# Kernel tuning notes

Hardware: AMD Instinct MI355X
Metric: run time of the kernel (lower is better)

## Reference

```python
import jax, jax.numpy as jnp
import numpy as np

N_NODES = 50000
N_EDGES = 500000
F = 128
AVG_DEG_LOG = float(np.log(11.0))  # log(avg_degree + 1), avg_degree = 10


def setup_inputs() -> dict:
    key = jax.random.key(0)
    ks = jax.random.split(key, 40)
    inp = {
        "x": jax.random.normal(ks[0], (N_NODES, F), dtype=jnp.float32),
        "edge_index": jax.random.randint(ks[1], (2, N_EDGES), 0, N_NODES, dtype=jnp.int32),
    }
    k = 2
    for i in range(5):
        inp[f"pre_w{i}"] = 0.05 * jax.random.normal(ks[k], (F, 2 * F), dtype=jnp.float32); k += 1
        inp[f"pre_b{i}"] = jnp.zeros((F,), jnp.float32)
        inp[f"adl{i}"] = jnp.full((1,), AVG_DEG_LOG, jnp.float32)
        inp[f"post_w{i}"] = 0.05 * jax.random.normal(ks[k], (F, 13 * F), dtype=jnp.float32); k += 1
        inp[f"post_b{i}"] = jnp.zeros((F,), jnp.float32)
        inp[f"lin_w{i}"] = 0.05 * jax.random.normal(ks[k], (F, F), dtype=jnp.float32); k += 1
        inp[f"lin_b{i}"] = jnp.zeros((F,), jnp.float32)
    return inp


def _pna_layer(x, src, dst, deg, adl, pre_w, pre_b, post_w, post_b, lin_w, lin_b):
    n = x.shape[0]
    # message: pre_nn(cat([x_i, x_j]))  -> [E, F]
    h = jnp.concatenate([x[dst], x[src]], axis=-1)        # [E, 2F]
    m = h @ pre_w.T + pre_b                               # [E, F]
    # multi-aggregator scatter-reduce onto target nodes
    inv = (1.0 / jnp.maximum(deg, 1.0))[:, None]
    mean = jax.ops.segment_sum(m, dst, num_segments=n) * inv
    mean2 = jax.ops.segment_sum(m * m, dst, num_segments=n) * inv
    std = jnp.sqrt(jnp.maximum(mean2 - mean * mean, 0.0) + 1e-5)
    has = (deg > 0)[:, None]
    mn = jnp.where(has, jax.ops.segment_min(m, dst, num_segments=n), 0.0)
    mx = jnp.where(has, jax.ops.segment_max(m, dst, num_segments=n), 0.0)
    agg = jnp.concatenate([mean, mn, mx, std], axis=-1)   # [N, 4F]
    # degree scalers: identity / amplification / attenuation
    scale = (jnp.log(jnp.maximum(deg, 1.0) + 1.0) / adl)[:, None]  # [N,1]
    out = jnp.concatenate([x, agg, agg * scale, agg / scale], axis=-1)  # [N, 13F]
    out = out @ post_w.T + post_b                          # [N, F]
    return out @ lin_w.T + lin_b                           # [N, F]


def reference(x, edge_index,
              pre_w0, pre_b0, adl0, post_w0, post_b0, lin_w0, lin_b0,
              pre_w1, pre_b1, adl1, post_w1, post_b1, lin_w1, lin_b1,
              pre_w2, pre_b2, adl2, post_w2, post_b2, lin_w2, lin_b2,
              pre_w3, pre_b3, adl3, post_w3, post_b3, lin_w3, lin_b3,
              pre_w4, pre_b4, adl4, post_w4, post_b4, lin_w4, lin_b4):
    src, dst = edge_index[0], edge_index[1]
    n = x.shape[0]
    deg = jax.ops.segment_sum(jnp.ones(src.shape[0], x.dtype), dst, num_segments=n)
    layers = [
        (pre_w0, pre_b0, adl0, post_w0, post_b0, lin_w0, lin_b0),
        (pre_w1, pre_b1, adl1, post_w1, post_b1, lin_w1, lin_b1),
        (pre_w2, pre_b2, adl2, post_w2, post_b2, lin_w2, lin_b2),
        (pre_w3, pre_b3, adl3, post_w3, post_b3, lin_w3, lin_b3),
        (pre_w4, pre_b4, adl4, post_w4, post_b4, lin_w4, lin_b4),
    ]
    h = x
    for pw, pb, adl, ow, ob, lw, lb in layers:
        h = _pna_layer(h, src, dst, deg, adl, pw, pb, ow, ob, lw, lb)
        h = jax.nn.relu(h)
    return h
```

## Files before the change

### kernel.cpp

```cpp
#include <hip/hip_runtime.h>

typedef short bf16x8 __attribute__((ext_vector_type(8)));
typedef float f32x4 __attribute__((ext_vector_type(4)));

struct Ptr5 { const float* p[5]; };
struct UPtr5 { unsigned char* p[5]; };
struct FPtr5 { float* p[5]; };

__device__ __forceinline__ unsigned short f2bf(float f) {
  unsigned u = __float_as_uint(f);
  u += 0x7fffu + ((u >> 16) & 1u);
  return (unsigned short)(u >> 16);
}

__device__ __forceinline__ float bf2f(unsigned short h) {
  return __uint_as_float(((unsigned)h) << 16);
}

__device__ __forceinline__ void gload16(const void* g, void* l) {
  __builtin_amdgcn_global_load_lds((const __attribute__((address_space(1))) void*)g,
                                   (__attribute__((address_space(3))) void*)l, 16, 0, 0);
}

__device__ __forceinline__ bf16x8 rf64(const unsigned char* lds, int row, int pb) {
  return *(const bf16x8*)(lds + row * 64 + (pb ^ ((((row) >> 1) & 3) << 4)));
}
__device__ __forceinline__ bf16x8 rf256(const unsigned char* lds, int row, int pb) {
  return *(const bf16x8*)(lds + row * 256 + (pb ^ ((row & 7) << 4)));
}

__global__ void k_hist(const int* __restrict__ dst, int* __restrict__ deg, int E) {
  int e = blockIdx.x * blockDim.x + threadIdx.x;
  if (e < E) atomicAdd(&deg[dst[e]], 1);
}

__global__ __launch_bounds__(256) void k_scan_part(const int* __restrict__ deg,
                                                    int* __restrict__ bsum, int n) {
  int b = blockIdx.x, t = threadIdx.x;
  int base = b * 1024 + t * 4;
  int s = 0;
#pragma unroll
  for (int i = 0; i < 4; i++) {
    int idx = base + i;
    if (idx < n) s += deg[idx];
  }
  for (int off = 1; off < 64; off <<= 1) s += __shfl_xor(s, off);
  __shared__ int ws[4];
  if ((t & 63) == 0) ws[t >> 6] = s;
  __syncthreads();
  if (t == 0) bsum[b] = ws[0] + ws[1] + ws[2] + ws[3];
}

__global__ void k_scan_bsum(const int* __restrict__ bsum, int* __restrict__ boff,
                            int* __restrict__ row_start, int nb, int n) {
  int t = threadIdx.x;
  int orig = (t < nb) ? bsum[t] : 0;
  int v = orig;
  for (int off = 1; off < 64; off <<= 1) {
    int u = __shfl_up(v, off);
    if (t >= off) v += u;
  }
  if (t < nb) boff[t] = v - orig;
  if (t == nb - 1) row_start[n] = v;
}

__global__ __launch_bounds__(256) void k_scan_final(const int* __restrict__ deg,
                                                     const int* __restrict__ boff,
                                                     int* __restrict__ row_start,
                                                     int* __restrict__ cursor, int n) {
  int b = blockIdx.x, t = threadIdx.x;
  int lane = t & 63, wid = t >> 6;
  int base = b * 1024 + t * 4;
  int v[4];
  int s = 0;
#pragma unroll
  for (int i = 0; i < 4; i++) {
    int idx = base + i;
    v[i] = (idx < n) ? deg[idx] : 0;
    s += v[i];
  }
  int sc = s;
  for (int off = 1; off < 64; off <<= 1) {
    int u = __shfl_up(sc, off);
    if (lane >= off) sc += u;
  }
  __shared__ int ws[4];
  if (lane == 63) ws[wid] = sc;
  __syncthreads();
  int wbase = 0;
  for (int i = 0; i < wid; i++) wbase += ws[i];
  int run = boff[b] + wbase + sc - s;
#pragma unroll
  for (int i = 0; i < 4; i++) {
    int idx = base + i;
    if (idx < n) {
      row_start[idx] = run;
      cursor[idx] = run;
      run += v[i];
    }
  }
}

__global__ void k_scatter(const int* __restrict__ src, const int* __restrict__ dst,
                          int* __restrict__ cursor, int* __restrict__ edge_src, int E) {
  int e = blockIdx.x * blockDim.x + threadIdx.x;
  if (e < E) {
    int pos = atomicAdd(&cursor[dst[e]], 1);
    edge_src[pos] = src[e];
  }
}

__global__ void k_cast(const float* __restrict__ x, unsigned short* __restrict__ X, int n) {
  int i = blockIdx.x * blockDim.x + threadIdx.x;
  if (i >= n * 32) return;
  int r = i >> 5, c = (i & 31) * 4;
  float4 v = *(const float4*)(x + (size_t)r * 128 + c);
  ushort4 o;
  o.x = f2bf(v.x); o.y = f2bf(v.y); o.z = f2bf(v.z); o.w = f2bf(v.w);
  *(ushort4*)(X + (size_t)r * 640 + c) = o;
}

__global__ __launch_bounds__(256) void k_fold5(Ptr5 post_w, Ptr5 pre_w, Ptr5 pre_b,
                                                Ptr5 post_b, float* __restrict__ Whg_base,
                                                FPtr5 biasg) {
  int L = blockIdx.y;
  int id = blockIdx.x * blockDim.x + threadIdx.x;
  if (id >= 3 * 128 * 128) return;
  int g = id >> 14;
  int rem = id & 16383;
  int j = rem >> 7, k = rem & 127;
  const float* pw = post_w.p[L] + j * 1664 + g * 512 + 128;
  const float* prw = pre_w.p[L];
  float acc = 0.f, bacc = 0.f;
  for (int f = 0; f < 128; f++) {
    float wc = pw[f] + pw[128 + f] + pw[256 + f];
    acc += wc * prw[f * 256 + k];
    if (k == 0) bacc += wc * pre_b.p[L][f];
  }
  Whg_base[L * 49152 + id] = acc;
  if (k == 0) biasg.p[L][g * 128 + j] = bacc + ((g == 0) ? post_b.p[L][j] : 0.f);
}

__global__ void k_repack_post5(Ptr5 post_w, const float* __restrict__ Whg_base, UPtr5 img) {
  int L = blockIdx.y;
  int i = blockIdx.x * blockDim.x + threadIdx.x;
  if (i >= 384 * 640) return;
  const float* pwL = post_w.p[L];
  const float* Whg = Whg_base + L * 49152;
  unsigned char* im = img.p[L];
  int r = i / 640, k = i - r * 640;
  int g = r >> 7, jj = r & 127;
  float v;
  if (k < 128) v = ((g == 0) ? pwL[jj * 1664 + k] : 0.0f) + Whg[(g * 128 + jj) * 128 + k];
  else v = pwL[jj * 1664 + g * 512 + 128 + (k - 128)];
  int kt = k >> 5, kl = k & 31;
  int ch = kl >> 3, e = kl & 7;
  int off = kt * 24576 + r * 64 + ((ch ^ ((r >> 1) & 3)) << 4) + e * 2;
  *(unsigned short*)(im + off) = f2bf(v);
}

__global__ void k_repack_ql5(Ptr5 pre_w, Ptr5 lin_w, UPtr5 qimg, UPtr5 limg) {
  int L = blockIdx.y;
  int which = blockIdx.z;
  int i = blockIdx.x * blockDim.x + threadIdx.x;
  if (i >= 128 * 128) return;
  int j = i >> 7, k = i & 127;
  float v = which ? lin_w.p[L][i] : pre_w.p[L][j * 256 + 128 + k];
  unsigned char* im = which ? limg.p[L] : qimg.p[L];
  int ch = k >> 3, e = k & 7;
  int off = j * 256 + ((ch * 16) ^ ((j & 7) << 4)) + e * 2;
  *(unsigned short*)(im + off) = f2bf(v);
}

__global__ __launch_bounds__(512, 2) void k_gemm1(const unsigned short* __restrict__ X,
                                                   const unsigned char* __restrict__ Qimg,
                                                   unsigned short* __restrict__ Qb) {
  __shared__ __align__(16) unsigned char lds[65536];
  int tid = threadIdx.x;
  int w = tid >> 6, lane = tid & 63;
  int wr = w >> 2, wc = w & 3;
  int l16 = lane & 15, lhi = lane >> 4;
  int row0 = blockIdx.x * 128;
  const char* Xb = (const char*)X;
#pragma unroll
  for (int j = 0; j < 4; j++) {
    int off = w * 4096 + j * 1024 + lane * 16;
    int r = off >> 8, pos = off & 255;
    int ch = (pos ^ ((r & 7) << 4)) >> 4;
    gload16(Xb + (size_t)(row0 + r) * 1280 + ch * 16, lds + w * 4096 + j * 1024);
  }
#pragma unroll
  for (int j = 0; j < 4; j++) {
    int off = w * 4096 + j * 1024;
    gload16(Qimg + off + lane * 16, lds + 32768 + off);
  }
  __syncthreads();
  f32x4 acc[4][2];
#pragma unroll
  for (int m = 0; m < 4; m++)
#pragma unroll
    for (int j = 0; j < 2; j++) acc[m][j] = (f32x4){0.f, 0.f, 0.f, 0.f};
#pragma unroll
  for (int ks = 0; ks < 4; ks++) {
    int pb = ks * 64 + lhi * 16;
    bf16x8 af[4], bfr[2];
#pragma unroll
    for (int m = 0; m < 4; m++) af[m] = rf256(lds, wr * 64 + m * 16 + l16, pb);
#pragma unroll
    for (int j = 0; j < 2; j++) bfr[j] = rf256(lds + 32768, wc * 32 + j * 16 + l16, pb);
#pragma unroll
    for (int m = 0; m < 4; m++)
#pragma unroll
      for (int j = 0; j < 2; j++)
        acc[m][j] = __builtin_amdgcn_mfma_f32_16x16x32_bf16(af[m], bfr[j], acc[m][j], 0, 0, 0);
  }
#pragma unroll
  for (int m = 0; m < 4; m++)
#pragma unroll
    for (int j = 0; j < 2; j++)
#pragma unroll
      for (int i = 0; i < 4; i++) {
        int r = row0 + wr * 64 + m * 16 + lhi * 4 + i;
        int c = wc * 32 + j * 16 + l16;
        Qb[(size_t)r * 128 + c] = f2bf(acc[m][j][i]);
      }
}

__global__ __launch_bounds__(256) void k_agg(const unsigned short* __restrict__ Qb,
                                              const int* __restrict__ row_start,
                                              const int* __restrict__ edge_src,
                                              const unsigned short* __restrict__ X_h,
                                              const float* __restrict__ pre_w,
                                              const float* __restrict__ pre_b,
                                              const float* __restrict__ adl,
                                              unsigned short* __restrict__ X,
                                              float* __restrict__ scale,
                                              float* __restrict__ inv_scale, int n) {
  int wv = (blockIdx.x * blockDim.x + threadIdx.x) >> 6;
  int lane = threadIdx.x & 63;
  int half = lane >> 5, fl = lane & 31;
  int v = 2 * wv + half;
  if (v >= n) return;
  int r0 = row_start[v], r1 = row_start[v + 1];
  int dg = r1 - r0;
  float mean[4], mnv[4], mxv[4], sdv[4];
  if (dg > 0) {
    float s[4] = {0.f, 0.f, 0.f, 0.f}, q[4] = {0.f, 0.f, 0.f, 0.f};
    float mn[4], mx[4];
#pragma unroll
    for (int t = 0; t < 4; t++) { mn[t] = INFINITY; mx[t] = -INFINITY; }
    const unsigned char* qbase = (const unsigned char*)Qb;
#define ACC4(U)                                                              \
  do {                                                                       \
    float f0 = __uint_as_float((U).x << 16);                                 \
    float f1 = __uint_as_float((U).x & 0xffff0000u);                         \
    float f2 = __uint_as_float((U).y << 16);                                 \
    float f3 = __uint_as_float((U).y & 0xffff0000u);                         \
    s[0] += f0; s[1] += f1; s[2] += f2; s[3] += f3;                          \
    q[0] += f0 * f0; q[1] += f1 * f1; q[2] += f2 * f2; q[3] += f3 * f3;      \
    mn[0] = fminf(mn[0], f0); mn[1] = fminf(mn[1], f1);                      \
    mn[2] = fminf(mn[2], f2); mn[3] = fminf(mn[3], f3);                      \
    mx[0] = fmaxf(mx[0], f0); mx[1] = fmaxf(mx[1], f1);                      \
    mx[2] = fmaxf(mx[2], f2); mx[3] = fmaxf(mx[3], f3);                      \
  } while (0)
    int e = r0;
    for (; e + 3 < r1; e += 4) {
      int sa = edge_src[e], sb = edge_src[e + 1], sc = edge_src[e + 2], sd = edge_src[e + 3];
      uint2 ua = *(const uint2*)(qbase + (size_t)sa * 256 + 8 * fl);
      uint2 ub = *(const uint2*)(qbase + (size_t)sb * 256 + 8 * fl);
      uint2 uc = *(const uint2*)(qbase + (size_t)sc * 256 + 8 * fl);
      uint2 ud = *(const uint2*)(qbase + (size_t)sd * 256 + 8 * fl);
      ACC4(ua); ACC4(ub); ACC4(uc); ACC4(ud);
    }
    for (; e < r1; e++) {
      int sa = edge_src[e];
      uint2 ua = *(const uint2*)(qbase + (size_t)sa * 256 + 8 * fl);
      ACC4(ua);
    }
#undef ACC4
    float invd = 1.0f / (float)dg;
#pragma unroll
    for (int t = 0; t < 4; t++) {
      mean[t] = s[t] * invd;
      float var = fmaxf(q[t] * invd - mean[t] * mean[t], 0.f);
      sdv[t] = sqrtf(var + 1e-5f);
      mnv[t] = mn[t]; mxv[t] = mx[t];
    }
  } else {
    const unsigned short* hv = X_h + (size_t)v * 640;
#pragma unroll
    for (int t = 0; t < 4; t++) {
      int j = 4 * fl + t;
      float c = pre_b[j];
      for (int k = 0; k < 128; k++) c += bf2f(hv[k]) * pre_w[j * 256 + k];
      mean[t] = mnv[t] = mxv[t] = -c;
      sdv[t] = sqrtf(1e-5f);
    }
  }
  unsigned short* row = X + (size_t)v * 640 + 128;
  ushort4 wm, wn, wx, ws;
  wm.x = f2bf(mean[0]); wm.y = f2bf(mean[1]); wm.z = f2bf(mean[2]); wm.w = f2bf(mean[3]);
  wn.x = f2bf(mnv[0]);  wn.y = f2bf(mnv[1]);  wn.z = f2bf(mnv[2]);  wn.w = f2bf(mnv[3]);
  wx.x = f2bf(mxv[0]);  wx.y = f2bf(mxv[1]);  wx.z = f2bf(mxv[2]);  wx.w = f2bf(mxv[3]);
  ws.x = f2bf(sdv[0]);  ws.y = f2bf(sdv[1]);  ws.z = f2bf(sdv[2]);  ws.w = f2bf(sdv[3]);
  *(ushort4*)(row + 4 * fl) = wm;
  *(ushort4*)(row + 128 + 4 * fl) = wn;
  *(ushort4*)(row + 256 + 4 * fl) = wx;
  *(ushort4*)(row + 384 + 4 * fl) = ws;
  if (fl == 0) {
    float degf = (float)dg;
    float sc = logf(fmaxf(degf, 1.0f) + 1.0f) / adl[0];
    scale[v] = sc;
    inv_scale[v] = 1.0f / sc;
  }
}

__global__ __launch_bounds__(512, 2) void k_fused(const unsigned short* __restrict__ X,
                                                   const unsigned char* __restrict__ Bimg,
                                                   const unsigned char* __restrict__ Limg,
                                                   const unsigned char* __restrict__ Qimg,
                                                   const float* __restrict__ scale,
                                                   const float* __restrict__ invs,
                                                   const float* __restrict__ biasg,
                                                   const float* __restrict__ lin_b,
                                                   unsigned short* __restrict__ Xh,
                                                   unsigned short* __restrict__ Qb,
                                                   float* __restrict__ Fout,
                                                   int M, int write_f32, int doC) {
  __shared__ __align__(16) unsigned char lds[65536];
  int tid = threadIdx.x;
  int w = tid >> 6, lane = tid & 63;
  int wr = w >> 2, wc = w & 3;
  int l16 = lane & 15, lhi = lane >> 4;
  int row0 = blockIdx.x * 128;
  const char* Xb = (const char*)X;
  int ra = tid >> 2;
  int posa = (((tid & 3) ^ ((ra >> 1) & 3)) << 4);
  const char* srcA = Xb + (size_t)(row0 + ra) * 1280 + posa;
  unsigned dstA = tid * 16;
  const unsigned char* srcB = Bimg + tid * 16;
  unsigned dstB = 8192 + tid * 16;

  f32x4 acc[4][6];
#pragma unroll
  for (int m = 0; m < 4; m++)
#pragma unroll
    for (int f = 0; f < 6; f++) acc[m][f] = (f32x4){0.f, 0.f, 0.f, 0.f};

#define STAGE_AB(buf, kt)                                                          \
  do {                                                                             \
    unsigned base = (buf) * 32768u;                                                \
    gload16(srcA + (kt) * 64, lds + base + dstA);                                  \
    _Pragma("unroll") for (int j = 0; j < 3; j++)                                  \
        gload16(srcB + (size_t)(kt) * 24576 + j * 8192, lds + base + dstB + j * 8192); \
  } while (0)

#define COMPUTE_A(buf)                                                             \
  do {                                                                             \
    const unsigned char* LA = lds + (buf) * 32768u;                                \
    const unsigned char* LB = LA + 8192;                                           \
    int pb = lhi * 16;                                                             \
    bf16x8 af[4], bfr[6];                                                          \
    _Pragma("unroll") for (int m = 0; m < 4; m++)                                  \
        af[m] = rf64(LA, wr * 64 + m * 16 + l16, pb);                              \
    _Pragma("unroll") for (int f = 0; f < 6; f++)                                  \
        bfr[f] = rf64(LB, (f >> 1) * 128 + wc * 32 + (f & 1) * 16 + l16, pb);      \
    _Pragma("unroll") for (int m = 0; m < 4; m++)                                  \
        _Pragma("unroll") for (int f = 0; f < 6; f++)                              \
            acc[m][f] =                                                            \
                __builtin_amdgcn_mfma_f32_16x16x32_bf16(af[m], bfr[f], acc[m][f], 0, 0, 0); \
  } while (0)

  STAGE_AB(0, 0);
  STAGE_AB(1, 1);
  for (int kt = 0; kt < 20; kt++) {
    if (kt < 19) {
      asm volatile("s_waitcnt vmcnt(4)" ::: "memory");
    } else {
      asm volatile("s_waitcnt vmcnt(0)" ::: "memory");
    }
    __builtin_amdgcn_s_barrier();
    __builtin_amdgcn_sched_barrier(0);
    __builtin_amdgcn_s_setprio(1);
    COMPUTE_A(kt & 1);
    __builtin_amdgcn_s_setprio(0);
    __builtin_amdgcn_sched_barrier(0);
    __builtin_amdgcn_s_barrier();
    if (kt < 18) STAGE_AB(kt & 1, kt + 2);
  }

#pragma unroll
  for (int j = 0; j < 4; j++) {
    int off = w * 4096 + j * 1024;
    gload16(Limg + off + lane * 16, lds + off);
  }
#pragma unroll
  for (int m = 0; m < 4; m++)
#pragma unroll
    for (int i = 0; i < 4; i++) {
      int rl = wr * 64 + m * 16 + lhi * 4 + i;
      int r = row0 + rl;
      float s = scale[r], iv = invs[r];
      int swz = (rl & 7) << 4;
#pragma unroll
      for (int j = 0; j < 2; j++) {
        int c = wc * 32 + j * 16 + l16;
        float v = acc[m][j][i] + s * acc[m][2 + j][i] + iv * acc[m][4 + j][i] + biasg[c] +
                  s * biasg[128 + c] + iv * biasg[256 + c];
        *(unsigned short*)(lds + 32768 + rl * 256 + ((2 * c) ^ swz)) = f2bf(v);
      }
    }
  __syncthreads();

  f32x4 acc2[4][2];
#pragma unroll
  for (int m = 0; m < 4; m++)
#pragma unroll
    for (int j = 0; j < 2; j++) acc2[m][j] = (f32x4){0.f, 0.f, 0.f, 0.f};
#pragma unroll
  for (int ks = 0; ks < 4; ks++) {
    int pb = ks * 64 + lhi * 16;
    bf16x8 af[4], bfr[2];
#pragma unroll
    for (int m = 0; m < 4; m++) af[m] = rf256(lds + 32768, wr * 64 + m * 16 + l16, pb);
#pragma unroll
    for (int j = 0; j < 2; j++) bfr[j] = rf256(lds, wc * 32 + j * 16 + l16, pb);
#pragma unroll
    for (int m = 0; m < 4; m++)
#pragma unroll
      for (int j = 0; j < 2; j++)
        acc2[m][j] = __builtin_amdgcn_mfma_f32_16x16x32_bf16(af[m], bfr[j], acc2[m][j], 0, 0, 0);
  }
  __syncthreads();

  if (doC) {
#pragma unroll
    for (int j = 0; j < 4; j++) {
      int off = w * 4096 + j * 1024;
      gload16(Qimg + off + lane * 16, lds + off);
    }
  }
#pragma unroll
  for (int m = 0; m < 4; m++)
#pragma unroll
    for (int j = 0; j < 2; j++)
#pragma unroll
      for (int i = 0; i < 4; i++) {
        int rl = wr * 64 + m * 16 + lhi * 4 + i;
        int r = row0 + rl;
        int c = wc * 32 + j * 16 + l16;
        float v = fmaxf(acc2[m][j][i] + lin_b[c], 0.0f);
        unsigned short hb = f2bf(v);
        Xh[(size_t)r * 640 + c] = hb;
        if (doC) *(unsigned short*)(lds + 32768 + rl * 256 + ((2 * c) ^ ((rl & 7) << 4))) = hb;
        if (write_f32 && r < M) Fout[(size_t)r * 128 + c] = v;
      }
  if (!doC) return;
  __syncthreads();

  f32x4 acc3[4][2];
#pragma unroll
  for (int m = 0; m < 4; m++)
#pragma unroll
    for (int j = 0; j < 2; j++) acc3[m][j] = (f32x4){0.f, 0.f, 0.f, 0.f};
#pragma unroll
  for (int ks = 0; ks < 4; ks++) {
    int pb = ks * 64 + lhi * 16;
    bf16x8 af[4], bfr[2];
#pragma unroll
    for (int m = 0; m < 4; m++) af[m] = rf256(lds + 32768, wr * 64 + m * 16 + l16, pb);
#pragma unroll
    for (int j = 0; j < 2; j++) bfr[j] = rf256(lds, wc * 32 + j * 16 + l16, pb);
#pragma unroll
    for (int m = 0; m < 4; m++)
#pragma unroll
      for (int j = 0; j < 2; j++)
        acc3[m][j] = __builtin_amdgcn_mfma_f32_16x16x32_bf16(af[m], bfr[j], acc3[m][j], 0, 0, 0);
  }
#pragma unroll
  for (int m = 0; m < 4; m++)
#pragma unroll
    for (int j = 0; j < 2; j++)
#pragma unroll
      for (int i = 0; i < 4; i++) {
        int r = row0 + wr * 64 + m * 16 + lhi * 4 + i;
        int c = wc * 32 + j * 16 + l16;
        Qb[(size_t)r * 128 + c] = f2bf(acc3[m][j][i]);
      }
#undef STAGE_AB
#undef COMPUTE_A
}

extern "C" void kernel_launch(void* const* d_in, const int* in_sizes, int n_in,
                              void* d_out, int out_size, void* d_ws, size_t ws_size,
                              hipStream_t stream) {
  const float* x = (const float*)d_in[0];
  const int* eidx = (const int*)d_in[1];
  int n = in_sizes[0] / 128;
  int E = in_sizes[1] / 2;
  int n_pad = (n + 127) & ~127;
  const int* src = eidx;
  const int* dst = eidx + E;

  Ptr5 pre_w, pre_b, adl, post_w, post_b, lin_w, lin_b;
  for (int i = 0; i < 5; i++) {
    pre_w.p[i] = (const float*)d_in[2 + i * 7 + 0];
    pre_b.p[i] = (const float*)d_in[2 + i * 7 + 1];
    adl.p[i] = (const float*)d_in[2 + i * 7 + 2];
    post_w.p[i] = (const float*)d_in[2 + i * 7 + 3];
    post_b.p[i] = (const float*)d_in[2 + i * 7 + 4];
    lin_w.p[i] = (const float*)d_in[2 + i * 7 + 5];
    lin_b.p[i] = (const float*)d_in[2 + i * 7 + 6];
  }

  char* ws = (char*)d_ws;
  size_t off = 0;
  auto alloc = [&](size_t bytes) {
    char* p = ws + off;
    off += (bytes + 255) & ~(size_t)255;
    return p;
  };
  unsigned short* X = (unsigned short*)alloc((size_t)n_pad * 640 * 2);
  unsigned short* Qb = (unsigned short*)alloc((size_t)n_pad * 128 * 2);
  float* scale = (float*)alloc((size_t)n_pad * 4);
  float* invs = (float*)alloc((size_t)n_pad * 4);
  int* deg = (int*)alloc((size_t)n * 4);
  int* row_start = (int*)alloc((size_t)(n + 1) * 4);
  int* cursor = (int*)alloc((size_t)n * 4);
  int* edge_src = (int*)alloc((size_t)E * 4);
  int nb = (n + 1023) / 1024;
  int* bsum = (int*)alloc((size_t)nb * 4);
  int* boff = (int*)alloc((size_t)nb * 4);
  float* Whg_base = (float*)alloc((size_t)5 * 3 * 128 * 128 * 4);
  UPtr5 Bpost, Lin, Qimg;
  FPtr5 biasg;
  for (int i = 0; i < 5; i++) {
    Bpost.p[i] = (unsigned char*)alloc(491520);
    Lin.p[i] = (unsigned char*)alloc(32768);
    Qimg.p[i] = (unsigned char*)alloc(32768);
    biasg.p[i] = (float*)alloc(384 * 4);
  }

  hipMemsetAsync(deg, 0, (size_t)n * 4, stream);
  k_hist<<<(E + 255) / 256, 256, 0, stream>>>(dst, deg, E);
  k_scan_part<<<nb, 256, 0, stream>>>(deg, bsum, n);
  k_scan_bsum<<<1, 64, 0, stream>>>(bsum, boff, row_start, nb, n);
  k_scan_final<<<nb, 256, 0, stream>>>(deg, boff, row_start, cursor, n);
  k_scatter<<<(E + 255) / 256, 256, 0, stream>>>(src, dst, cursor, edge_src, E);
  k_cast<<<(n * 32 + 255) / 256, 256, 0, stream>>>(x, X, n);
  k_fold5<<<dim3(192, 5), 256, 0, stream>>>(post_w, pre_w, pre_b, post_b, Whg_base, biasg);
  k_repack_post5<<<dim3(960, 5), 256, 0, stream>>>(post_w, Whg_base, Bpost);
  k_repack_ql5<<<dim3(64, 5, 2), 256, 0, stream>>>(pre_w, lin_w, Qimg, Lin);

  int gblocks = n_pad / 128;
  k_gemm1<<<gblocks, 512, 0, stream>>>(X, Qimg.p[0], Qb);
  for (int L = 0; L < 5; L++) {
    k_agg<<<(n + 7) / 8, 256, 0, stream>>>(Qb, row_start, edge_src, X, pre_w.p[L], pre_b.p[L],
                                           adl.p[L], X, scale, invs, n);
    k_fused<<<gblocks, 512, 0, stream>>>(X, Bpost.p[L], Lin.p[L],
                                         (L < 4) ? Qimg.p[L + 1] : Qimg.p[0], scale, invs,
                                         biasg.p[L], lin_b.p[L], X, Qb, (float*)d_out, n,
                                         (L == 4) ? 1 : 0, (L < 4) ? 1 : 0);
  }
}
```

Measured before the change: 501.6 us.

## Load GEMM operands directly from global into registers, repacking B per-lane

Replaces the LDS double-buffered global_load_lds pipeline in the fused kernel's main GEMM with direct per-lane global loads of A and B fragments into registers. It removes the barriers, waitcnts and LDS traffic. The post-weight image is re-laid out so that each lane's 16-byte B fragment is contiguous in MFMA-fragment order. The trade-off is that B is no longer shared through LDS: every wave reloads its fragments from global/L2, and there is no explicit prefetch to hide latency.

After: 665.8 us. +32.7%, slower.

```diff
diff --git a/kernel.cpp b/kernel.cpp
--- a/kernel.cpp
+++ b/kernel.cpp
@@ -22,9 +22,6 @@
                                    (__attribute__((address_space(3))) void*)l, 16, 0, 0);
 }
 
-__device__ __forceinline__ bf16x8 rf64(const unsigned char* lds, int row, int pb) {
-  return *(const bf16x8*)(lds + row * 64 + (pb ^ ((((row) >> 1) & 3) << 4)));
-}
 __device__ __forceinline__ bf16x8 rf256(const unsigned char* lds, int row, int pb) {
   return *(const bf16x8*)(lds + row * 256 + (pb ^ ((row & 7) << 4)));
 }
@@ -145,18 +142,22 @@
   int L = blockIdx.y;
   int i = blockIdx.x * blockDim.x + threadIdx.x;
   if (i >= 384 * 640) return;
-  const float* pwL = post_w.p[L];
+  int chunk = i >> 9;
+  int rem = i & 511;
+  int f = chunk % 6;
+  int wcc = (chunk / 6) & 3;
+  int kt = chunk / 24;
+  int l16 = rem >> 5;
+  int lhi = (rem >> 3) & 3;
+  int e = rem & 7;
+  int row = (f >> 1) * 128 + wcc * 32 + (f & 1) * 16 + l16;
+  int k = kt * 32 + lhi * 8 + e;
+  int g = row >> 7, jj = row & 127;
   const float* Whg = Whg_base + L * 49152;
-  unsigned char* im = img.p[L];
-  int r = i / 640, k = i - r * 640;
-  int g = r >> 7, jj = r & 127;
   float v;
-  if (k < 128) v = ((g == 0) ? pwL[jj * 1664 + k] : 0.0f) + Whg[(g * 128 + jj) * 128 + k];
-  else v = pwL[jj * 1664 + g * 512 + 128 + (k - 128)];
-  int kt = k >> 5, kl = k & 31;
-  int ch = kl >> 3, e = kl & 7;
-  int off = kt * 24576 + r * 64 + ((ch ^ ((r >> 1) & 3)) << 4) + e * 2;
-  *(unsigned short*)(im + off) = f2bf(v);
+  if (k < 128) v = ((g == 0) ? post_w.p[L][jj * 1664 + k] : 0.0f) + Whg[(g * 128 + jj) * 128 + k];
+  else v = post_w.p[L][jj * 1664 + g * 512 + 128 + (k - 128)];
+  ((unsigned short*)img.p[L])[i] = f2bf(v);
 }
 
 __global__ void k_repack_ql5(Ptr5 pre_w, Ptr5 lin_w, UPtr5 qimg, UPtr5 limg) {
@@ -333,13 +334,13 @@
   int wr = w >> 2, wc = w & 3;
   int l16 = lane & 15, lhi = lane >> 4;
   int row0 = blockIdx.x * 128;
-  const char* Xb = (const char*)X;
-  int ra = tid >> 2;
-  int posa = (((tid & 3) ^ ((ra >> 1) & 3)) << 4);
-  const char* srcA = Xb + (size_t)(row0 + ra) * 1280 + posa;
-  unsigned dstA = tid * 16;
-  const unsigned char* srcB = Bimg + tid * 16;
-  unsigned dstB = 8192 + tid * 16;
+  const unsigned char* Xb = (const unsigned char*)X;
+
+  const unsigned char* Ab[4];
+#pragma unroll
+  for (int m = 0; m < 4; m++)
+    Ab[m] = Xb + (size_t)(row0 + wr * 64 + m * 16 + l16) * 1280 + lhi * 16;
+  const unsigned char* Bb = Bimg + wc * 6144 + l16 * 64 + lhi * 16;
 
   f32x4 acc[4][6];
 #pragma unroll
@@ -347,46 +348,18 @@
 #pragma unroll
     for (int f = 0; f < 6; f++) acc[m][f] = (f32x4){0.f, 0.f, 0.f, 0.f};
 
-#define STAGE_AB(buf, kt)                                                          \
-  do {                                                                             \
-    unsigned base = (buf) * 32768u;                                                \
-    gload16(srcA + (kt) * 64, lds + base + dstA);                                  \
-    _Pragma("unroll") for (int j = 0; j < 3; j++)                                  \
-        gload16(srcB + (size_t)(kt) * 24576 + j * 8192, lds + base + dstB + j * 8192); \
-  } while (0)
-
-#define COMPUTE_A(buf)                                                             \
-  do {                                                                             \
-    const unsigned char* LA = lds + (buf) * 32768u;                                \
-    const unsigned char* LB = LA + 8192;                                           \
-    int pb = lhi * 16;                                                             \
-    bf16x8 af[4], bfr[6];                                                          \
-    _Pragma("unroll") for (int m = 0; m < 4; m++)                                  \
-        af[m] = rf64(LA, wr * 64 + m * 16 + l16, pb);                              \
-    _Pragma("unroll") for (int f = 0; f < 6; f++)                                  \
-        bfr[f] = rf64(LB, (f >> 1) * 128 + wc * 32 + (f & 1) * 16 + l16, pb);      \
-    _Pragma("unroll") for (int m = 0; m < 4; m++)                                  \
-        _Pragma("unroll") for (int f = 0; f < 6; f++)                              \
-            acc[m][f] =                                                            \
-                __builtin_amdgcn_mfma_f32_16x16x32_bf16(af[m], bfr[f], acc[m][f], 0, 0, 0); \
-  } while (0)
-
-  STAGE_AB(0, 0);
-  STAGE_AB(1, 1);
+#pragma unroll
   for (int kt = 0; kt < 20; kt++) {
-    if (kt < 19) {
-      asm volatile("s_waitcnt vmcnt(4)" ::: "memory");
-    } else {
-      asm volatile("s_waitcnt vmcnt(0)" ::: "memory");
-    }
-    __builtin_amdgcn_s_barrier();
-    __builtin_amdgcn_sched_barrier(0);
-    __builtin_amdgcn_s_setprio(1);
-    COMPUTE_A(kt & 1);
-    __builtin_amdgcn_s_setprio(0);
-    __builtin_amdgcn_sched_barrier(0);
-    __builtin_amdgcn_s_barrier();
-    if (kt < 18) STAGE_AB(kt & 1, kt + 2);
+    bf16x8 af[4], bfr[6];
+#pragma unroll
+    for (int m = 0; m < 4; m++) af[m] = *(const bf16x8*)(Ab[m] + kt * 64);
+#pragma unroll
+    for (int f = 0; f < 6; f++) bfr[f] = *(const bf16x8*)(Bb + kt * 24576 + f * 1024);
+#pragma unroll
+    for (int m = 0; m < 4; m++)
+#pragma unroll
+      for (int f = 0; f < 6; f++)
+        acc[m][f] = __builtin_amdgcn_mfma_f32_16x16x32_bf16(af[m], bfr[f], acc[m][f], 0, 0, 0);
   }
 
 #pragma unroll
@@ -487,8 +460,6 @@
         int c = wc * 32 + j * 16 + l16;
         Qb[(size_t)r * 128 + c] = f2bf(acc3[m][j][i]);
       }
-#undef STAGE_AB
-#undef COMPUTE_A
 }
 
 extern "C" void kernel_launch(void* const* d_in, const int* in_sizes, int n_in,
```
